# Optimization experiments

Hardware: AMD Instinct MI355X
Metric: run time of the kernel (lower is better)

Reference implementation:

```python
import jax, jax.numpy as jnp
import numpy as np
from jax import lax

B, CIN, S = 16, 1, 64          # batch, input channels, spatial
C = 16                          # c_out hidden channels
T = 50                          # ODE steps
DT = 0.5
NC = 7                          # n_classes
K = T // 2 + 1                  # rfft bins = 26
HID = 256


def conv2d_same(x, w, b):
    # x:(B,Ci,H,W) w:(Co,Ci,3,3) zero 'SAME' padding (torch padding=1)
    y = lax.conv_general_dilated(x, w, (1, 1), 'SAME',
                                 dimension_numbers=('NCHW', 'OIHW', 'NCHW'))
    return y + b[None, :, None, None]


def conv2d_circular(x, w):
    # circular padding=1, no bias (coRNNCell.Wy)
    xp = jnp.pad(x, ((0, 0), (0, 0), (1, 1), (1, 1)), mode='wrap')
    return lax.conv_general_dilated(xp, w, (1, 1), 'VALID',
                                    dimension_numbers=('NCHW', 'OIHW', 'NCHW'))


def setup_inputs() -> dict:
    key = jax.random.key(0)
    ks = iter(jax.random.split(key, 40))
    d = {}
    d['x'] = jax.random.normal(next(ks), (B, CIN, S, S), dtype=jnp.float32)

    def cw(ci, co):
        return jax.random.normal(next(ks), (co, ci, 3, 3), jnp.float32) * (1.0 / np.sqrt(ci * 9))

    # omega / alpha encoders: 3 convs each
    for p in ('om', 'al'):
        d[f'{p}_w1'], d[f'{p}_b1'] = cw(CIN, C), jnp.zeros((C,), jnp.float32)
        d[f'{p}_w2'], d[f'{p}_b2'] = cw(C, C), jnp.zeros((C,), jnp.float32)
        d[f'{p}_w3'], d[f'{p}_b3'] = cw(C, C), jnp.zeros((C,), jnp.float32)
    # hy encoder: 4 convs
    d['hy_w1'], d['hy_b1'] = cw(CIN, C), jnp.zeros((C,), jnp.float32)
    d['hy_w2'], d['hy_b2'] = cw(C, C), jnp.zeros((C,), jnp.float32)
    d['hy_w3'], d['hy_b3'] = cw(C, C), jnp.zeros((C,), jnp.float32)
    d['hy_w4'], d['hy_b4'] = cw(C, C), jnp.zeros((C,), jnp.float32)
    # cell conv: block-diagonal discrete Laplacian (per torch init)
    lap = np.array([[0., 1., 0.], [1., -4., 1.], [0., 1., 0.]], np.float32)
    wy = np.zeros((C, C, 3, 3), np.float32)
    wy[np.arange(C), np.arange(C)] = lap
    d['wy'] = jnp.asarray(wy)
    # readout MLP: 416 -> 256 -> 256 -> 256 -> 7
    dims = [K * C, HID, HID, HID, NC]
    for i in range(4):
        d[f'ro_w{i+1}'] = jax.random.normal(next(ks), (dims[i], dims[i + 1]), jnp.float32) * (1.0 / np.sqrt(dims[i]))
        d[f'ro_b{i+1}'] = jnp.zeros((dims[i + 1],), jnp.float32)
    return d


def _forward(x,
             om_w1, om_b1, om_w2, om_b2, om_w3, om_b3,
             al_w1, al_b1, al_w2, al_b2, al_w3, al_b3,
             hy_w1, hy_b1, hy_w2, hy_b2, hy_w3, hy_b3, hy_w4, hy_b4,
             wy,
             ro_w1, ro_b1, ro_w2, ro_b2, ro_w3, ro_b3, ro_w4, ro_b4):
    relu = jax.nn.relu
    # encoders
    om = relu(conv2d_same(relu(conv2d_same(relu(conv2d_same(x, om_w1, om_b1)), om_w2, om_b2)), om_w3, om_b3))
    al = relu(conv2d_same(relu(conv2d_same(relu(conv2d_same(x, al_w1, al_b1)), al_w2, al_b2)), al_w3, al_b3))
    h = relu(conv2d_same(x, hy_w1, hy_b1))
    h = relu(conv2d_same(h, hy_w2, hy_b2))
    h = relu(conv2d_same(h, hy_w3, hy_b3))
    hy0 = jnp.tanh(conv2d_same(h, hy_w4, hy_b4))

    omega = om.reshape(B, C, S * S)
    alpha = al.reshape(B, C, S * S)
    hy = hy0.reshape(B, C, S * S)
    hz = jnp.zeros_like(hy)

    def step(carry, _):
        hy, hz = carry
        sf = jnp.tanh(conv2d_circular(hy.reshape(B, C, S, S), wy)).reshape(B, C, S * S)
        new_hz = hz + DT * (sf - omega * hy - alpha * hz)
        new_hy = hy + DT * new_hz
        return (new_hy, new_hz), new_hy

    _, y_seq = lax.scan(step, (hy, hz), None, length=T)   # (T,B,C,HW)
    y_seq = jnp.transpose(y_seq, (1, 3, 2, 0)).reshape(B * S * S, C, T)  # (BHW,C,T)

    fft_mag = jnp.abs(jnp.fft.rfft(y_seq, axis=2))        # (BHW,C,K)
    f = fft_mag.reshape(B * S * S, C * K)                  # (BHW, C*K)

    f = relu(f @ ro_w1 + ro_b1)
    f = relu(f @ ro_w2 + ro_b2)
    f = relu(f @ ro_w3 + ro_b3)
    logits_flat = f @ ro_w4 + ro_b4                        # (BHW, NC)
    logits = logits_flat.reshape(B, S, S, NC).transpose(0, 3, 1, 2)
    return logits


def reference(x,
              om_w1, om_b1, om_w2, om_b2, om_w3, om_b3,
              al_w1, al_b1, al_w2, al_b2, al_w3, al_b3,
              hy_w1, hy_b1, hy_w2, hy_b2, hy_w3, hy_b3, hy_w4, hy_b4,
              wy,
              ro_w1, ro_b1, ro_w2, ro_b2, ro_w3, ro_b3, ro_w4, ro_b4):
    return _forward(x,
                    om_w1, om_b1, om_w2, om_b2, om_w3, om_b3,
                    al_w1, al_b1, al_w2, al_b2, al_w3, al_b3,
                    hy_w1, hy_b1, hy_w2, hy_b2, hy_w3, hy_b3, hy_w4, hy_b4,
                    wy,
                    ro_w1, ro_b1, ro_w2, ro_b2, ro_w3, ro_b3, ro_w4, ro_b4)
```

## Files before the change

kernel.cpp:

```cpp
#include <hip/hip_runtime.h>
#include <hip/hip_bf16.h>
#include <hip/hip_fp16.h>
#include <math.h>

#define B_   16
#define C_   16
#define S_   64
#define HW_  4096
#define T_   50
#define K_   26
#define F_   416
#define HID_ 256
#define NC_  7
#define DT_  0.5f
#define BCHW_ (B_*C_*HW_)
#define M_   (B_*HW_)

typedef _Float16 f16x8  __attribute__((ext_vector_type(8)));
typedef __fp16   fp16x2 __attribute__((ext_vector_type(2)));
typedef float    f32x4  __attribute__((ext_vector_type(4)));
typedef float    f32x2  __attribute__((ext_vector_type(2)));

__device__ __forceinline__ void gld_lds16(const void* g, void* l){
    __builtin_amdgcn_global_load_lds(
        (const __attribute__((address_space(1))) void*)g,
        (__attribute__((address_space(3))) void*)l, 16, 0, 0);
}

__device__ __forceinline__ float fast_tanh(float x){
    float ax = fabsf(x);
    float e  = __expf(2.f*ax);
    float r  = 1.f - 2.f/(e + 1.f);
    return copysignf(r, x);
}

__device__ __forceinline__ short f2h_s(float f){
    __half h = __float2half(f);
    return *(short*)&h;
}

template<int CIN, int ACT>
__global__ __launch_bounds__(256) void convf_kernel(
    const float* __restrict__ in0, const float* __restrict__ in1, const float* __restrict__ in2,
    const float* __restrict__ w0,  const float* __restrict__ w1,  const float* __restrict__ w2,
    const float* __restrict__ b0,  const float* __restrict__ b1,  const float* __restrict__ b2,
    float* __restrict__ o0, float* __restrict__ o1, float* __restrict__ o2)
{
    __shared__ __align__(16) float slab[CIN][10][66];
    const int slice = blockIdx.x;
    const int b     = blockIdx.y;
    const int ch    = blockIdx.z;
    const float* in = (ch == 0) ? in0 : (ch == 1) ? in1 : in2;
    const float* w  = (ch == 0) ? w0  : (ch == 1) ? w1  : w2;
    const float* bb = (ch == 0) ? b0  : (ch == 1) ? b1  : b2;
    float* out      = (ch == 0) ? o0  : (ch == 1) ? o1  : o2;

    const int tid = threadIdx.x;
    const int y0  = slice * 8;

    for (int idx = tid; idx < CIN*10*66; idx += 256){
        int ci  = idx / (10*66);
        int rem = idx % (10*66);
        int rr  = rem / 66;
        int cc  = rem % 66;
        int gy = y0 - 1 + rr;
        int gx = cc - 1;
        float v = 0.f;
        if ((unsigned)gy < 64u && (unsigned)gx < 64u)
            v = in[(size_t)(b*CIN + ci)*HW_ + gy*64 + gx];
        slab[ci][rr][cc] = v;
    }
    __syncthreads();

    const int x2 = (tid & 31) * 2;
    const int ry = tid >> 5;

    f32x2 acc[16];
    #pragma unroll
    for (int co = 0; co < 16; co++) acc[co] = (f32x2){bb[co], bb[co]};

    for (int ci = 0; ci < CIN; ci++){
        f32x2 p[3][3];
        #pragma unroll
        for (int dy = 0; dy < 3; dy++){
            float s0 = slab[ci][ry + dy][x2 + 0];
            float s1 = slab[ci][ry + dy][x2 + 1];
            float s2 = slab[ci][ry + dy][x2 + 2];
            float s3 = slab[ci][ry + dy][x2 + 3];
            p[dy][0] = (f32x2){s0, s1};
            p[dy][1] = (f32x2){s1, s2};
            p[dy][2] = (f32x2){s2, s3};
        }
        #pragma unroll
        for (int co = 0; co < 16; co++){
            const float* wp = w + (size_t)(co*CIN + ci)*9;
            f32x2 s = acc[co];
            #pragma unroll
            for (int dy = 0; dy < 3; dy++)
                #pragma unroll
                for (int dx = 0; dx < 3; dx++){
                    float wc = wp[dy*3 + dx];
                    s += (f32x2){wc, wc} * p[dy][dx];
                }
            acc[co] = s;
        }
    }
    #pragma unroll
    for (int co = 0; co < 16; co++){
        float v0 = acc[co].x, v1 = acc[co].y;
        if (ACT){ v0 = fast_tanh(v0); v1 = fast_tanh(v1); }
        else    { v0 = fmaxf(v0, 0.f); v1 = fmaxf(v1, 0.f); }
        *(float2*)&out[(size_t)(b*16 + co)*HW_ + (y0 + ry)*64 + x2] =
            make_float2(v0, v1);
    }
}

__global__ __launch_bounds__(1024) void ode_kernel(
    const float* __restrict__ omega, const float* __restrict__ alpha,
    const float* __restrict__ hy0,   const float* __restrict__ wy,
    __half* __restrict__ yseq)
{
    __shared__ __align__(16) float buf[2][64*68];
    const int blk = blockIdx.x;
    const int c   = blk & 15;
    const int tid = threadIdx.x;
    const int y   = tid >> 4;
    const int xq  = (tid & 15) << 2;
    const size_t off = (size_t)blk * HW_;
    const int g0  = y*64 + xq;

    float4 om4 = *(const float4*)(omega + off + g0);
    float4 al4 = *(const float4*)(alpha + off + g0);
    float4 h4  = *(const float4*)(hy0   + off + g0);

    f32x2 om2[2] = { (f32x2){DT_*om4.x, DT_*om4.y}, (f32x2){DT_*om4.z, DT_*om4.w} };
    f32x2 al2[2] = { (f32x2){1.f - DT_*al4.x, 1.f - DT_*al4.y},
                     (f32x2){1.f - DT_*al4.z, 1.f - DT_*al4.w} };
    f32x2 hz2[2] = { (f32x2){0.f, 0.f}, (f32x2){0.f, 0.f} };
    float hv[4]  = { h4.x, h4.y, h4.z, h4.w };
    *(float4*)&buf[0][y*68 + xq] = h4;

    float wv[9];
    const float* wp = wy + (size_t)(c*C_ + c)*9;
    #pragma unroll
    for (int j = 0; j < 9; j++) wv[j] = wp[j];
    const bool five = (wv[0]==0.f) & (wv[2]==0.f) & (wv[6]==0.f) & (wv[8]==0.f);
    const f32x2 w1v = (f32x2){wv[1], wv[1]};
    const f32x2 w3v = (f32x2){wv[3], wv[3]};
    const f32x2 w4v = (f32x2){wv[4], wv[4]};
    const f32x2 w5v = (f32x2){wv[5], wv[5]};
    const f32x2 w7v = (f32x2){wv[7], wv[7]};
    const f32x2 dt2 = (f32x2){DT_, DT_};
    __syncthreads();

    const int ym = ((y + 63) & 63) * 68;
    const int yp = ((y + 1)  & 63) * 68;
    const int yo = y * 68;
    const int xm = (xq + 63) & 63;
    const int xp = (xq + 4)  & 63;
    const __half* ybase = yseq + off + g0;

    int cur = 0;
    for (int t = 0; t < T_; t++){
        const float* hp = buf[cur];
        float* hn = buf[cur ^ 1];
        float4 up4 = *(const float4*)&hp[ym + xq];
        float4 dn4 = *(const float4*)&hp[yp + xq];
        float lft = hp[yo + xm];
        float rgt = hp[yo + xp];

        float ny0, ny1, ny2, ny3;
        if (five){
            f32x2 u0 = (f32x2){up4.x, up4.y}, u1 = (f32x2){up4.z, up4.w};
            f32x2 d0 = (f32x2){dn4.x, dn4.y}, d1 = (f32x2){dn4.z, dn4.w};
            f32x2 c0 = (f32x2){hv[0], hv[1]}, c1 = (f32x2){hv[2], hv[3]};
            f32x2 l0 = (f32x2){lft,  hv[0]};
            f32x2 l1 = (f32x2){hv[1], hv[2]};
            f32x2 r1 = (f32x2){hv[3], rgt};

            f32x2 s0 = w4v*c0 + w1v*u0 + w7v*d0 + w3v*l0 + w5v*l1;
            f32x2 s1 = w4v*c1 + w1v*u1 + w7v*d1 + w3v*l1 + w5v*r1;

            f32x2 sf0 = (f32x2){fast_tanh(s0.x), fast_tanh(s0.y)};
            f32x2 sf1 = (f32x2){fast_tanh(s1.x), fast_tanh(s1.y)};

            f32x2 nz0 = al2[0]*hz2[0] - om2[0]*c0 + dt2*sf0;
            f32x2 nz1 = al2[1]*hz2[1] - om2[1]*c1 + dt2*sf1;
            f32x2 nyv0 = dt2*nz0 + c0;
            f32x2 nyv1 = dt2*nz1 + c1;
            hz2[0] = nz0; hz2[1] = nz1;
            ny0 = nyv0.x; ny1 = nyv0.y; ny2 = nyv1.x; ny3 = nyv1.y;
        } else {
            float upv[4] = {up4.x, up4.y, up4.z, up4.w};
            float dnv[4] = {dn4.x, dn4.y, dn4.z, dn4.w};
            float ul = hp[ym + xm], ur = hp[ym + xp];
            float dl = hp[yp + xm], dr = hp[yp + xp];
            float hzl[4] = {hz2[0].x, hz2[0].y, hz2[1].x, hz2[1].y};
            float oml[4] = {om2[0].x, om2[0].y, om2[1].x, om2[1].y};
            float all[4] = {al2[0].x, al2[0].y, al2[1].x, al2[1].y};
            float nyv[4];
            #pragma unroll
            for (int i = 0; i < 4; i++){
                float l  = (i == 0) ? lft : hv[i-1];
                float r  = (i == 3) ? rgt : hv[i+1];
                float uL = (i == 0) ? ul  : upv[i-1];
                float uR = (i == 3) ? ur  : upv[i+1];
                float dL = (i == 0) ? dl  : dnv[i-1];
                float dR = (i == 3) ? dr  : dnv[i+1];
                float s = wv[0]*uL + wv[1]*upv[i] + wv[2]*uR
                        + wv[3]*l  + wv[4]*hv[i]  + wv[5]*r
                        + wv[6]*dL + wv[7]*dnv[i] + wv[8]*dR;
                float sf = fast_tanh(s);
                float nz = fmaf(all[i], hzl[i], fmaf(-oml[i], hv[i], DT_*sf));
                nyv[i] = fmaf(DT_, nz, hv[i]);
                hzl[i] = nz;
            }
            hz2[0] = (f32x2){hzl[0], hzl[1]};
            hz2[1] = (f32x2){hzl[2], hzl[3]};
            ny0 = nyv[0]; ny1 = nyv[1]; ny2 = nyv[2]; ny3 = nyv[3];
        }

        hv[0] = ny0; hv[1] = ny1; hv[2] = ny2; hv[3] = ny3;
        *(float4*)&hn[yo + xq] = make_float4(ny0, ny1, ny2, ny3);

        union { fp16x2 h2[2]; uint2 u; } pk;
        pk.h2[0] = __builtin_amdgcn_cvt_pkrtz(ny0, ny1);
        pk.h2[1] = __builtin_amdgcn_cvt_pkrtz(ny2, ny3);
        *(uint2*)(ybase + (size_t)t*BCHW_) = pk.u;

        __syncthreads();
        cur ^= 1;
    }
}

__global__ __launch_bounds__(256) void dft_mfma_kernel(
    const __half* __restrict__ yseq, __half* __restrict__ f)
{
    __shared__ __align__(16) char Ys[8*256*16];
    __shared__ __align__(16) char Gs[8*64*16];
    const int tid = threadIdx.x;
    const int blk = blockIdx.x;
    const int bc  = blk >> 4;
    const int p0  = (blk & 15) << 8;
    const int b   = bc >> 4, c = bc & 15;

    for (int idx = tid; idx < 64*64; idx += 256){
        int r = idx >> 6, t = idx & 63;
        float v = 0.f;
        if (r < 52 && t < 50){
            int k  = r >> 1;
            int ph = (k * t) % 50;
            float ang = (float)ph * (6.2831853071795864f / 50.f);
            v = (r & 1) ? __sinf(ang) : __cosf(ang);
        }
        *(_Float16*)(Gs + ((t >> 3)*64 + r)*16 + (t & 7)*2) = (_Float16)v;
    }

    {
        const __half* src = yseq + (size_t)bc*HW_ + p0 + tid;
        #pragma unroll
        for (int t2 = 0; t2 < 25; t2++){
            unsigned int a = *(const unsigned short*)&src[(size_t)(2*t2)*BCHW_];
            unsigned int d = *(const unsigned short*)&src[(size_t)(2*t2+1)*BCHW_];
            int t8 = t2 >> 2, j = t2 & 3;
            *(unsigned int*)(Ys + (t8*256 + tid)*16 + j*4) = a | (d << 16);
        }
        #pragma unroll
        for (int t2 = 25; t2 < 32; t2++){
            int t8 = t2 >> 2, j = t2 & 3;
            *(unsigned int*)(Ys + (t8*256 + tid)*16 + j*4) = 0u;
        }
    }
    __syncthreads();

    const int lane = tid & 63;
    const int w    = tid >> 6;
    const int n    = lane & 15;
    const int quad = lane >> 4;
    const int mrow = 16*w + n;

    f16x8 a0 = *(const f16x8*)(Gs + ((quad    )*64 + mrow)*16);
    f16x8 a1 = *(const f16x8*)(Gs + ((quad + 4)*64 + mrow)*16);

    const int kb0   = 8*w + 2*quad;
    const bool valid = (kb0 < K_);

    for (int nt = 0; nt < 16; nt++){
        f16x8 b0 = *(const f16x8*)(Ys + ((quad    )*256 + nt*16 + n)*16);
        f16x8 b1 = *(const f16x8*)(Ys + ((quad + 4)*256 + nt*16 + n)*16);
        f32x4 acc = (f32x4){0.f, 0.f, 0.f, 0.f};
        acc = __builtin_amdgcn_mfma_f32_16x16x32_f16(a0, b0, acc, 0, 0, 0);
        acc = __builtin_amdgcn_mfma_f32_16x16x32_f16(a1, b1, acc, 0, 0, 0);
        if (valid){
            float m0 = sqrtf(fmaf(acc[0], acc[0], acc[1]*acc[1]));
            float m1 = sqrtf(fmaf(acc[2], acc[2], acc[3]*acc[3]));
            unsigned int u = ((unsigned int)(unsigned short)f2h_s(m1) << 16)
                           |  (unsigned int)(unsigned short)f2h_s(m0);
            const int row = b*HW_ + p0 + nt*16 + n;
            *(unsigned int*)((char*)(f + (size_t)row*F_ + c*K_) + kb0*2) = u;
        }
    }
}

__global__ __launch_bounds__(256) void prep_all_kernel(
    const float* __restrict__ w1, const float* __restrict__ w2,
    const float* __restrict__ w3,
    __half* __restrict__ wt1, __half* __restrict__ wt2, __half* __restrict__ wt3)
{
    const int blk = blockIdx.x;
    const int tid = threadIdx.x;
    if (blk < 256){
        const int n = blk;
        for (int k = tid; k < F_; k += 256)
            wt1[(size_t)n*F_ + k] = __float2half(w1[(size_t)k*HID_ + n]);
    } else if (blk < 512){
        const int n = blk - 256;
        for (int k = tid; k < HID_; k += 256)
            wt2[(size_t)n*HID_ + k] = __float2half(w2[(size_t)k*HID_ + n]);
    } else {
        const int n = blk - 512;
        for (int k = tid; k < HID_; k += 256)
            wt3[(size_t)n*HID_ + k] = __float2half(w3[(size_t)k*HID_ + n]);
    }
}

__global__ __launch_bounds__(512, 2) void mlp_fused_kernel(
    const __half* __restrict__ A,
    const __half* __restrict__ Wt1,
    const __half* __restrict__ Wt2,
    const __half* __restrict__ Wt3,
    const float* __restrict__ b1, const float* __restrict__ b2,
    const float* __restrict__ b3,
    const float* __restrict__ w4, const float* __restrict__ b4,
    float* __restrict__ out)
{
    __shared__ __align__(16) short hbuf[256*264];
    __shared__ __align__(16) short Bs[4*2064];
    __shared__ __align__(16) short Bs4[512*8];

    const int tid  = threadIdx.x;
    const int lane = tid & 63;
    const int wave = tid >> 6;
    const int wm   = (wave & 3) * 64;
    const int wn   = (wave >> 2) * 128;
    const int n16  = lane & 15;
    const int quad = lane >> 4;
    const int m0   = blockIdx.x * 256;

    {
        const int ktq = tid >> 4, n = tid & 15;
        short vals[8];
        #pragma unroll
        for (int e = 0; e < 8; e++){
            const int k = ktq*8 + e;
            vals[e] = f2h_s((n < NC_) ? w4[(size_t)k*NC_ + n] : 0.f);
        }
        #pragma unroll
        for (int e = 0; e < 8; e++) Bs4[tid*8 + e] = vals[e];
    }

    const int id0 = tid, id1 = tid + 512;
    const int kc0 = id0 >> 8, nn0 = id0 & 255;
    const int kc1 = id1 >> 8, nn1 = id1 & 255;
    char* dst0 = (char*)Bs + kc0*4128 + nn0*16;
    char* dst1 = (char*)Bs + kc1*4128 + nn1*16;

    f32x4 acc[4][8];
    #pragma unroll
    for (int i = 0; i < 4; i++)
        #pragma unroll
        for (int j = 0; j < 8; j++)
            acc[i][j] = (f32x4){0.f,0.f,0.f,0.f};

    const __half* arow[4];
    #pragma unroll
    for (int i = 0; i < 4; i++)
        arow[i] = A + (size_t)(m0 + wm + i*16 + n16)*F_ + quad*8;

    f16x8 afn[4];
    #pragma unroll
    for (int i = 0; i < 4; i++) afn[i] = *(const f16x8*)(arow[i]);

    for (int k0 = 0; k0 < F_; k0 += 32){
        gld_lds16(Wt1 + (size_t)nn0*F_ + k0 + kc0*8, dst0);
        gld_lds16(Wt1 + (size_t)nn1*F_ + k0 + kc1*8, dst1);
        __syncthreads();
        f16x8 af[4];
        #pragma unroll
        for (int i = 0; i < 4; i++) af[i] = afn[i];
        if (k0 + 32 < F_){
            #pragma unroll
            for (int i = 0; i < 4; i++) afn[i] = *(const f16x8*)(arow[i] + k0 + 32);
        }
        f16x8 bf[8];
        #pragma unroll
        for (int j = 0; j < 8; j++)
            bf[j] = *(const f16x8*)((char*)Bs + quad*4128 + (wn + j*16 + n16)*16);
        #pragma unroll
        for (int i = 0; i < 4; i++)
            #pragma unroll
            for (int j = 0; j < 8; j++)
                acc[i][j] = __builtin_amdgcn_mfma_f32_16x16x32_f16(
                                af[i], bf[j], acc[i][j], 0, 0, 0);
        __syncthreads();
    }
    #pragma unroll
    for (int j = 0; j < 8; j++){
        const int col = wn + j*16 + n16;
        const float bv = b1[col];
        #pragma unroll
        for (int i = 0; i < 4; i++){
            const int r0 = wm + i*16 + quad*4;
            #pragma unroll
            for (int r = 0; r < 4; r++)
                hbuf[(r0 + r)*264 + col] = f2h_s(fmaxf(acc[i][j][r] + bv, 0.f));
        }
    }
    __syncthreads();

    const __half* Wts[2] = {Wt2, Wt3};
    const float* bls[2] = {b2, b3};
    for (int L = 0; L < 2; L++){
        const __half* Wt = Wts[L];
        #pragma unroll
        for (int i = 0; i < 4; i++)
            #pragma unroll
            for (int j = 0; j < 8; j++)
                acc[i][j] = (f32x4){0.f,0.f,0.f,0.f};

        for (int k0 = 0; k0 < HID_; k0 += 32){
            gld_lds16(Wt + (size_t)nn0*HID_ + k0 + kc0*8, dst0);
            gld_lds16(Wt + (size_t)nn1*HID_ + k0 + kc1*8, dst1);
            f16x8 af[4];
            #pragma unroll
            for (int i = 0; i < 4; i++)
                af[i] = *(const f16x8*)&hbuf[(wm + i*16 + n16)*264 + k0 + quad*8];
            __syncthreads();
            f16x8 bf[8];
            #pragma unroll
            for (int j = 0; j < 8; j++)
                bf[j] = *(const f16x8*)((char*)Bs + quad*4128 + (wn + j*16 + n16)*16);
            #pragma unroll
            for (int i = 0; i < 4; i++)
                #pragma unroll
                for (int j = 0; j < 8; j++)
                    acc[i][j] = __builtin_amdgcn_mfma_f32_16x16x32_f16(
                                    af[i], bf[j], acc[i][j], 0, 0, 0);
            __syncthreads();
        }
        const float* bl = bls[L];
        #pragma unroll
        for (int j = 0; j < 8; j++){
            const int col = wn + j*16 + n16;
            const float bv = bl[col];
            #pragma unroll
            for (int i = 0; i < 4; i++){
                const int r0 = wm + i*16 + quad*4;
                #pragma unroll
                for (int r = 0; r < 4; r++)
                    hbuf[(r0 + r)*264 + col] = f2h_s(fmaxf(acc[i][j][r] + bv, 0.f));
            }
        }
        __syncthreads();
    }

    f32x4 facc[2] = {(f32x4){0.f,0.f,0.f,0.f}, (f32x4){0.f,0.f,0.f,0.f}};
    #pragma unroll
    for (int kt = 0; kt < 8; kt++){
        f16x8 bfr = *(const f16x8*)&Bs4[((kt*4 + quad)*16 + n16)*8];
        #pragma unroll
        for (int mt = 0; mt < 2; mt++){
            f16x8 af = *(const f16x8*)&hbuf[(wave*32 + mt*16 + n16)*264 + kt*32 + quad*8];
            facc[mt] = __builtin_amdgcn_mfma_f32_16x16x32_f16(af, bfr, facc[mt], 0, 0, 0);
        }
    }
    if (n16 < NC_){
        const float bv = b4[n16];
        #pragma unroll
        for (int mt = 0; mt < 2; mt++){
            #pragma unroll
            for (int r = 0; r < 4; r++){
                const int grow = m0 + wave*32 + mt*16 + quad*4 + r;
                const int bidx = grow >> 12, hw = grow & 4095;
                out[(size_t)(bidx*NC_ + n16)*HW_ + hw] = facc[mt][r] + bv;
            }
        }
    }
}

extern "C" void kernel_launch(void* const* d_in, const int* in_sizes, int n_in,
                              void* d_out, int out_size, void* d_ws, size_t ws_size,
                              hipStream_t stream)
{
    const float* x     = (const float*)d_in[0];
    const float* om_w1 = (const float*)d_in[1];  const float* om_b1 = (const float*)d_in[2];
    const float* om_w2 = (const float*)d_in[3];  const float* om_b2 = (const float*)d_in[4];
    const float* om_w3 = (const float*)d_in[5];  const float* om_b3 = (const float*)d_in[6];
    const float* al_w1 = (const float*)d_in[7];  const float* al_b1 = (const float*)d_in[8];
    const float* al_w2 = (const float*)d_in[9];  const float* al_b2 = (const float*)d_in[10];
    const float* al_w3 = (const float*)d_in[11]; const float* al_b3 = (const float*)d_in[12];
    const float* hy_w1 = (const float*)d_in[13]; const float* hy_b1 = (const float*)d_in[14];
    const float* hy_w2 = (const float*)d_in[15]; const float* hy_b2 = (const float*)d_in[16];
    const float* hy_w3 = (const float*)d_in[17]; const float* hy_b3 = (const float*)d_in[18];
    const float* hy_w4 = (const float*)d_in[19]; const float* hy_b4 = (const float*)d_in[20];
    const float* wy    = (const float*)d_in[21];
    const float* ro_w1 = (const float*)d_in[22]; const float* ro_b1 = (const float*)d_in[23];
    const float* ro_w2 = (const float*)d_in[24]; const float* ro_b2 = (const float*)d_in[25];
    const float* ro_w3 = (const float*)d_in[26]; const float* ro_b3 = (const float*)d_in[27];
    const float* ro_w4 = (const float*)d_in[28]; const float* ro_b4 = (const float*)d_in[29];
    float* out = (float*)d_out;

    char* wsb = (char*)d_ws;
    const size_t YSEQ_BYTES = (size_t)T_ * BCHW_ * 2;
    __half* yseq = (__half*)wsb;
    __half* fbuf = (__half*)(wsb + YSEQ_BYTES);

    const size_t MB4 = (size_t)BCHW_ * 4;
    float* om_t1 = (float*)(wsb + YSEQ_BYTES + 0*MB4);
    float* al_t1 = (float*)(wsb + YSEQ_BYTES + 1*MB4);
    float* hy_t1 = (float*)(wsb + YSEQ_BYTES + 2*MB4);
    float* om_t2 = (float*)(wsb + YSEQ_BYTES + 3*MB4);
    float* al_t2 = (float*)(wsb + YSEQ_BYTES + 4*MB4);
    float* hy_t2 = (float*)(wsb + YSEQ_BYTES + 5*MB4);
    float* omega = (float*)(wsb + YSEQ_BYTES + 6*MB4);
    float* alpha = (float*)(wsb + YSEQ_BYTES + 7*MB4);
    float* hy_t3 = (float*)(wsb + YSEQ_BYTES + 8*MB4);
    float* hy0   = (float*)(wsb + YSEQ_BYTES + 9*MB4);

    __half* wt1 = (__half*)(wsb + 0);
    __half* wt2 = (__half*)(wsb + 212992);
    __half* wt3 = (__half*)(wsb + 344064);

    convf_kernel<1,0><<<dim3(8,B_,3), 256, 0, stream>>>(
        x, x, x, om_w1, al_w1, hy_w1, om_b1, al_b1, hy_b1, om_t1, al_t1, hy_t1);
    convf_kernel<16,0><<<dim3(8,B_,3), 256, 0, stream>>>(
        om_t1, al_t1, hy_t1, om_w2, al_w2, hy_w2, om_b2, al_b2, hy_b2, om_t2, al_t2, hy_t2);
    convf_kernel<16,0><<<dim3(8,B_,3), 256, 0, stream>>>(
        om_t2, al_t2, hy_t2, om_w3, al_w3, hy_w3, om_b3, al_b3, hy_b3, omega, alpha, hy_t3);
    convf_kernel<16,1><<<dim3(8,B_,1), 256, 0, stream>>>(
        hy_t3, hy_t3, hy_t3, hy_w4, hy_w4, hy_w4, hy_b4, hy_b4, hy_b4, hy0, hy0, hy0);
    ode_kernel<<<256, 1024, 0, stream>>>(omega, alpha, hy0, wy, yseq);
    dft_mfma_kernel<<<4096, 256, 0, stream>>>(yseq, fbuf);
    prep_all_kernel<<<768, 256, 0, stream>>>(ro_w1, ro_w2, ro_w3, wt1, wt2, wt3);
    mlp_fused_kernel<<<256, 512, 0, stream>>>(
        fbuf, wt1, wt2, wt3, ro_b1, ro_b2, ro_b3, ro_w4, ro_b4, out);
}
```

Before: 372.1 us.

## Shrink fused MLP tile to 64 rows, 4 waves, XOR-swizzled LDS

Reworks the fused MLP kernel from 256-row tiles with 8 waves to 64-row tiles with 4 waves, launching 1024 blocks instead of 256 so all CUs are busy. The hidden-activation buffer is shrunk and uses an XOR swizzle in place of row padding to avoid LDS bank conflicts, and the final-layer weights now reuse the B staging buffer. The trade-off is that each block reloads the full weight matrices, so there is four times as much weight traffic through L2 and less reuse per weight tile.

```diff
diff --git a/kernel.cpp b/kernel.cpp
--- a/kernel.cpp
+++ b/kernel.cpp
@@ -324,7 +324,7 @@
     }
 }
 
-__global__ __launch_bounds__(512, 2) void mlp_fused_kernel(
+__global__ __launch_bounds__(256, 3) void mlp_fused_kernel(
     const __half* __restrict__ A,
     const __half* __restrict__ Wt1,
     const __half* __restrict__ Wt2,
@@ -334,56 +334,45 @@
     const float* __restrict__ w4, const float* __restrict__ b4,
     float* __restrict__ out)
 {
-    __shared__ __align__(16) short hbuf[256*264];
-    __shared__ __align__(16) short Bs[4*2064];
-    __shared__ __align__(16) short Bs4[512*8];
+    __shared__ __align__(16) short hbuf[64*256];
+    __shared__ __align__(16) short Bs[1024*8];
 
     const int tid  = threadIdx.x;
     const int lane = tid & 63;
     const int wave = tid >> 6;
-    const int wm   = (wave & 3) * 64;
-    const int wn   = (wave >> 2) * 128;
+    const int wn   = wave * 64;
     const int n16  = lane & 15;
     const int quad = lane >> 4;
-    const int m0   = blockIdx.x * 256;
-
-    {
-        const int ktq = tid >> 4, n = tid & 15;
-        short vals[8];
-        #pragma unroll
-        for (int e = 0; e < 8; e++){
-            const int k = ktq*8 + e;
-            vals[e] = f2h_s((n < NC_) ? w4[(size_t)k*NC_ + n] : 0.f);
-        }
-        #pragma unroll
-        for (int e = 0; e < 8; e++) Bs4[tid*8 + e] = vals[e];
-    }
-
-    const int id0 = tid, id1 = tid + 512;
-    const int kc0 = id0 >> 8, nn0 = id0 & 255;
-    const int kc1 = id1 >> 8, nn1 = id1 & 255;
-    char* dst0 = (char*)Bs + kc0*4128 + nn0*16;
-    char* dst1 = (char*)Bs + kc1*4128 + nn1*16;
-
-    f32x4 acc[4][8];
+    const int m0   = blockIdx.x * 64;
+
+    int kcs[4], nns[4];
+    #pragma unroll
+    for (int s = 0; s < 4; s++){
+        int id = tid + 256*s;
+        kcs[s] = id >> 8; nns[s] = id & 255;
+    }
+
+    f32x4 acc[4][4];
     #pragma unroll
     for (int i = 0; i < 4; i++)
         #pragma unroll
-        for (int j = 0; j < 8; j++)
+        for (int j = 0; j < 4; j++)
             acc[i][j] = (f32x4){0.f,0.f,0.f,0.f};
 
     const __half* arow[4];
     #pragma unroll
     for (int i = 0; i < 4; i++)
-        arow[i] = A + (size_t)(m0 + wm + i*16 + n16)*F_ + quad*8;
+        arow[i] = A + (size_t)(m0 + i*16 + n16)*F_ + quad*8;
 
     f16x8 afn[4];
     #pragma unroll
     for (int i = 0; i < 4; i++) afn[i] = *(const f16x8*)(arow[i]);
 
     for (int k0 = 0; k0 < F_; k0 += 32){
-        gld_lds16(Wt1 + (size_t)nn0*F_ + k0 + kc0*8, dst0);
-        gld_lds16(Wt1 + (size_t)nn1*F_ + k0 + kc1*8, dst1);
+        #pragma unroll
+        for (int s = 0; s < 4; s++)
+            gld_lds16(Wt1 + (size_t)nns[s]*F_ + k0 + kcs[s]*8,
+                      (char*)Bs + (tid + 256*s)*16);
         __syncthreads();
         f16x8 af[4];
         #pragma unroll
@@ -392,28 +381,31 @@
             #pragma unroll
             for (int i = 0; i < 4; i++) afn[i] = *(const f16x8*)(arow[i] + k0 + 32);
         }
-        f16x8 bf[8];
-        #pragma unroll
-        for (int j = 0; j < 8; j++)
-            bf[j] = *(const f16x8*)((char*)Bs + quad*4128 + (wn + j*16 + n16)*16);
+        f16x8 bf[4];
+        #pragma unroll
+        for (int j = 0; j < 4; j++)
+            bf[j] = *(const f16x8*)&Bs[(quad*256 + wn + j*16 + n16)*8];
         #pragma unroll
         for (int i = 0; i < 4; i++)
             #pragma unroll
-            for (int j = 0; j < 8; j++)
+            for (int j = 0; j < 4; j++)
                 acc[i][j] = __builtin_amdgcn_mfma_f32_16x16x32_f16(
                                 af[i], bf[j], acc[i][j], 0, 0, 0);
         __syncthreads();
     }
     #pragma unroll
-    for (int j = 0; j < 8; j++){
+    for (int j = 0; j < 4; j++){
         const int col = wn + j*16 + n16;
         const float bv = b1[col];
         #pragma unroll
         for (int i = 0; i < 4; i++){
-            const int r0 = wm + i*16 + quad*4;
-            #pragma unroll
-            for (int r = 0; r < 4; r++)
-                hbuf[(r0 + r)*264 + col] = f2h_s(fmaxf(acc[i][j][r] + bv, 0.f));
+            const int r0 = i*16 + quad*4;
+            #pragma unroll
+            for (int r = 0; r < 4; r++){
+                const int row = r0 + r;
+                hbuf[row*256 + (((col>>3) ^ (row&7))<<3) + (col&7)] =
+                    f2h_s(fmaxf(acc[i][j][r] + bv, 0.f));
+            }
         }
     }
     __syncthreads();
@@ -425,65 +417,80 @@
         #pragma unroll
         for (int i = 0; i < 4; i++)
             #pragma unroll
-            for (int j = 0; j < 8; j++)
+            for (int j = 0; j < 4; j++)
                 acc[i][j] = (f32x4){0.f,0.f,0.f,0.f};
 
         for (int k0 = 0; k0 < HID_; k0 += 32){
-            gld_lds16(Wt + (size_t)nn0*HID_ + k0 + kc0*8, dst0);
-            gld_lds16(Wt + (size_t)nn1*HID_ + k0 + kc1*8, dst1);
+            #pragma unroll
+            for (int s = 0; s < 4; s++)
+                gld_lds16(Wt + (size_t)nns[s]*HID_ + k0 + kcs[s]*8,
+                          (char*)Bs + (tid + 256*s)*16);
             f16x8 af[4];
             #pragma unroll
-            for (int i = 0; i < 4; i++)
-                af[i] = *(const f16x8*)&hbuf[(wm + i*16 + n16)*264 + k0 + quad*8];
+            for (int i = 0; i < 4; i++){
+                const int row = i*16 + n16;
+                const int phys = ((k0>>3) + quad) ^ (row & 7);
+                af[i] = *(const f16x8*)&hbuf[row*256 + phys*8];
+            }
             __syncthreads();
-            f16x8 bf[8];
-            #pragma unroll
-            for (int j = 0; j < 8; j++)
-                bf[j] = *(const f16x8*)((char*)Bs + quad*4128 + (wn + j*16 + n16)*16);
+            f16x8 bf[4];
+            #pragma unroll
+            for (int j = 0; j < 4; j++)
+                bf[j] = *(const f16x8*)&Bs[(quad*256 + wn + j*16 + n16)*8];
             #pragma unroll
             for (int i = 0; i < 4; i++)
                 #pragma unroll
-                for (int j = 0; j < 8; j++)
+                for (int j = 0; j < 4; j++)
                     acc[i][j] = __builtin_amdgcn_mfma_f32_16x16x32_f16(
                                     af[i], bf[j], acc[i][j], 0, 0, 0);
             __syncthreads();
         }
         const float* bl = bls[L];
         #pragma unroll
-        for (int j = 0; j < 8; j++){
+        for (int j = 0; j < 4; j++){
             const int col = wn + j*16 + n16;
             const float bv = bl[col];
             #pragma unroll
             for (int i = 0; i < 4; i++){
-                const int r0 = wm + i*16 + quad*4;
+                const int r0 = i*16 + quad*4;
                 #pragma unroll
-                for (int r = 0; r < 4; r++)
-                    hbuf[(r0 + r)*264 + col] = f2h_s(fmaxf(acc[i][j][r] + bv, 0.f));
+                for (int r = 0; r < 4; r++){
+                    const int row = r0 + r;
+                    hbuf[row*256 + (((col>>3) ^ (row&7))<<3) + (col&7)] =
+                        f2h_s(fmaxf(acc[i][j][r] + bv, 0.f));
+                }
             }
         }
         __syncthreads();
     }
 
-    f32x4 facc[2] = {(f32x4){0.f,0.f,0.f,0.f}, (f32x4){0.f,0.f,0.f,0.f}};
+    #pragma unroll
+    for (int s = 0; s < 2; s++){
+        const int id  = tid + 256*s;
+        const int ktq = id >> 4, nn4 = id & 15;
+        #pragma unroll
+        for (int e = 0; e < 8; e++)
+            Bs[id*8 + e] = f2h_s((nn4 < NC_) ?
+                w4[(size_t)(ktq*8 + e)*NC_ + nn4] : 0.f);
+    }
+    __syncthreads();
+
+    f32x4 facc = (f32x4){0.f,0.f,0.f,0.f};
+    const int frow = wave*16 + n16;
     #pragma unroll
     for (int kt = 0; kt < 8; kt++){
-        f16x8 bfr = *(const f16x8*)&Bs4[((kt*4 + quad)*16 + n16)*8];
-        #pragma unroll
-        for (int mt = 0; mt < 2; mt++){
-            f16x8 af = *(const f16x8*)&hbuf[(wave*32 + mt*16 + n16)*264 + kt*32 + quad*8];
-            facc[mt] = __builtin_amdgcn_mfma_f32_16x16x32_f16(af, bfr, facc[mt], 0, 0, 0);
-        }
+        f16x8 bfr = *(const f16x8*)&Bs[((kt*4 + quad)*16 + n16)*8];
+        const int phys = (kt*4 + quad) ^ (frow & 7);
+        f16x8 af = *(const f16x8*)&hbuf[frow*256 + phys*8];
+        facc = __builtin_amdgcn_mfma_f32_16x16x32_f16(af, bfr, facc, 0, 0, 0);
     }
     if (n16 < NC_){
         const float bv = b4[n16];
         #pragma unroll
-        for (int mt = 0; mt < 2; mt++){
-            #pragma unroll
-            for (int r = 0; r < 4; r++){
-                const int grow = m0 + wave*32 + mt*16 + quad*4 + r;
-                const int bidx = grow >> 12, hw = grow & 4095;
-                out[(size_t)(bidx*NC_ + n16)*HW_ + hw] = facc[mt][r] + bv;
-            }
+        for (int r = 0; r < 4; r++){
+            const int grow = m0 + wave*16 + quad*4 + r;
+            const int bidx = grow >> 12, hw = grow & 4095;
+            out[(size_t)(bidx*NC_ + n16)*HW_ + hw] = facc[r] + bv;
         }
     }
 }
@@ -542,6 +549,6 @@
     ode_kernel<<<256, 1024, 0, stream>>>(omega, alpha, hy0, wy, yseq);
     dft_mfma_kernel<<<4096, 256, 0, stream>>>(yseq, fbuf);
     prep_all_kernel<<<768, 256, 0, stream>>>(ro_w1, ro_w2, ro_w3, wt1, wt2, wt3);
-    mlp_fused_kernel<<<256, 512, 0, stream>>>(
+    mlp_fused_kernel<<<1024, 256, 0, stream>>>(
         fbuf, wt1, wt2, wt3, ro_b1, ro_b2, ro_b3, ro_w4, ro_b4, out);
 }
```

Measured after the change: 422.7 us. +13.6%, slower.

## Double K-step per barrier in fused MLP and XOR-swizzle hidden buffer

Applied to the files above, without the earlier changes.

The fused MLP kernel now processes 64 K-elements per LDS stage (two MFMA k-substeps per pair of barriers) instead of 32, which halves the number of barrier pairs in each layer. The padded hidden buffer (row stride 264) is replaced by an unpadded 256-stride buffer with an XOR swizzle to avoid LDS bank conflicts. The separate W4 staging buffer is removed and W4 is loaded into the reused B buffer only after layer 3, which cuts the kernel's LDS footprint. In exchange, the A-operand software prefetch is dropped and there is a peeled tail step for K=416.

```diff
diff --git a/kernel.cpp b/kernel.cpp
--- a/kernel.cpp
+++ b/kernel.cpp
@@ -334,9 +334,8 @@
     const float* __restrict__ w4, const float* __restrict__ b4,
     float* __restrict__ out)
 {
-    __shared__ __align__(16) short hbuf[256*264];
-    __shared__ __align__(16) short Bs[4*2064];
-    __shared__ __align__(16) short Bs4[512*8];
+    __shared__ __align__(16) short hbuf[256*256];
+    __shared__ __align__(16) short Bs[8*256*8];
 
     const int tid  = threadIdx.x;
     const int lane = tid & 63;
@@ -347,23 +346,12 @@
     const int quad = lane >> 4;
     const int m0   = blockIdx.x * 256;
 
-    {
-        const int ktq = tid >> 4, n = tid & 15;
-        short vals[8];
-        #pragma unroll
-        for (int e = 0; e < 8; e++){
-            const int k = ktq*8 + e;
-            vals[e] = f2h_s((n < NC_) ? w4[(size_t)k*NC_ + n] : 0.f);
-        }
-        #pragma unroll
-        for (int e = 0; e < 8; e++) Bs4[tid*8 + e] = vals[e];
-    }
-
-    const int id0 = tid, id1 = tid + 512;
-    const int kc0 = id0 >> 8, nn0 = id0 & 255;
-    const int kc1 = id1 >> 8, nn1 = id1 & 255;
-    char* dst0 = (char*)Bs + kc0*4128 + nn0*16;
-    char* dst1 = (char*)Bs + kc1*4128 + nn1*16;
+    int kcs[4], nns[4];
+    #pragma unroll
+    for (int s = 0; s < 4; s++){
+        int id = tid + 512*s;
+        kcs[s] = id >> 8; nns[s] = id & 255;
+    }
 
     f32x4 acc[4][8];
     #pragma unroll
@@ -377,25 +365,50 @@
     for (int i = 0; i < 4; i++)
         arow[i] = A + (size_t)(m0 + wm + i*16 + n16)*F_ + quad*8;
 
-    f16x8 afn[4];
-    #pragma unroll
-    for (int i = 0; i < 4; i++) afn[i] = *(const f16x8*)(arow[i]);
-
-    for (int k0 = 0; k0 < F_; k0 += 32){
-        gld_lds16(Wt1 + (size_t)nn0*F_ + k0 + kc0*8, dst0);
-        gld_lds16(Wt1 + (size_t)nn1*F_ + k0 + kc1*8, dst1);
+    for (int k0 = 0; k0 < 384; k0 += 64){
+        #pragma unroll
+        for (int s = 0; s < 4; s++)
+            gld_lds16(Wt1 + (size_t)nns[s]*F_ + k0 + kcs[s]*8,
+                      (char*)Bs + (tid + 512*s)*16);
+        f16x8 af[2][4];
+        #pragma unroll
+        for (int h = 0; h < 2; h++)
+            #pragma unroll
+            for (int i = 0; i < 4; i++)
+                af[h][i] = *(const f16x8*)(arow[i] + k0 + h*32);
         __syncthreads();
+        #pragma unroll
+        for (int h = 0; h < 2; h++){
+            f16x8 bf[8];
+            #pragma unroll
+            for (int j = 0; j < 8; j++)
+                bf[j] = *(const f16x8*)&Bs[((h*4 + quad)*256 + wn + j*16 + n16)*8];
+            #pragma unroll
+            for (int i = 0; i < 4; i++)
+                #pragma unroll
+                for (int j = 0; j < 8; j++)
+                    acc[i][j] = __builtin_amdgcn_mfma_f32_16x16x32_f16(
+                                    af[h][i], bf[j], acc[i][j], 0, 0, 0);
+        }
+        __syncthreads();
+    }
+    {
+        const int k0 = 384;
+        #pragma unroll
+        for (int s = 0; s < 2; s++){
+            int id = tid + 512*s;
+            int kc = id >> 8;
+            int nn = id & 255;
+            gld_lds16(Wt1 + (size_t)nn*F_ + k0 + kc*8, (char*)Bs + id*16);
+        }
         f16x8 af[4];
         #pragma unroll
-        for (int i = 0; i < 4; i++) af[i] = afn[i];
-        if (k0 + 32 < F_){
-            #pragma unroll
-            for (int i = 0; i < 4; i++) afn[i] = *(const f16x8*)(arow[i] + k0 + 32);
-        }
+        for (int i = 0; i < 4; i++) af[i] = *(const f16x8*)(arow[i] + k0);
+        __syncthreads();
         f16x8 bf[8];
         #pragma unroll
         for (int j = 0; j < 8; j++)
-            bf[j] = *(const f16x8*)((char*)Bs + quad*4128 + (wn + j*16 + n16)*16);
+            bf[j] = *(const f16x8*)&Bs[(quad*256 + wn + j*16 + n16)*8];
         #pragma unroll
         for (int i = 0; i < 4; i++)
             #pragma unroll
@@ -412,8 +425,11 @@
         for (int i = 0; i < 4; i++){
             const int r0 = wm + i*16 + quad*4;
             #pragma unroll
-            for (int r = 0; r < 4; r++)
-                hbuf[(r0 + r)*264 + col] = f2h_s(fmaxf(acc[i][j][r] + bv, 0.f));
+            for (int r = 0; r < 4; r++){
+                const int row = r0 + r;
+                hbuf[row*256 + (((col>>3) ^ (row&7))<<3) + (col&7)] =
+                    f2h_s(fmaxf(acc[i][j][r] + bv, 0.f));
+            }
         }
     }
     __syncthreads();
@@ -428,24 +444,34 @@
             for (int j = 0; j < 8; j++)
                 acc[i][j] = (f32x4){0.f,0.f,0.f,0.f};
 
-        for (int k0 = 0; k0 < HID_; k0 += 32){
-            gld_lds16(Wt + (size_t)nn0*HID_ + k0 + kc0*8, dst0);
-            gld_lds16(Wt + (size_t)nn1*HID_ + k0 + kc1*8, dst1);
-            f16x8 af[4];
-            #pragma unroll
-            for (int i = 0; i < 4; i++)
-                af[i] = *(const f16x8*)&hbuf[(wm + i*16 + n16)*264 + k0 + quad*8];
+        for (int k0 = 0; k0 < HID_; k0 += 64){
+            #pragma unroll
+            for (int s = 0; s < 4; s++)
+                gld_lds16(Wt + (size_t)nns[s]*HID_ + k0 + kcs[s]*8,
+                          (char*)Bs + (tid + 512*s)*16);
+            f16x8 af[2][4];
+            #pragma unroll
+            for (int h = 0; h < 2; h++)
+                #pragma unroll
+                for (int i = 0; i < 4; i++){
+                    const int row  = wm + i*16 + n16;
+                    const int phys = ((k0>>3) + h*4 + quad) ^ (row & 7);
+                    af[h][i] = *(const f16x8*)&hbuf[row*256 + phys*8];
+                }
             __syncthreads();
-            f16x8 bf[8];
-            #pragma unroll
-            for (int j = 0; j < 8; j++)
-                bf[j] = *(const f16x8*)((char*)Bs + quad*4128 + (wn + j*16 + n16)*16);
-            #pragma unroll
-            for (int i = 0; i < 4; i++)
+            #pragma unroll
+            for (int h = 0; h < 2; h++){
+                f16x8 bf[8];
                 #pragma unroll
                 for (int j = 0; j < 8; j++)
-                    acc[i][j] = __builtin_amdgcn_mfma_f32_16x16x32_f16(
-                                    af[i], bf[j], acc[i][j], 0, 0, 0);
+                    bf[j] = *(const f16x8*)&Bs[((h*4 + quad)*256 + wn + j*16 + n16)*8];
+                #pragma unroll
+                for (int i = 0; i < 4; i++)
+                    #pragma unroll
+                    for (int j = 0; j < 8; j++)
+                        acc[i][j] = __builtin_amdgcn_mfma_f32_16x16x32_f16(
+                                        af[h][i], bf[j], acc[i][j], 0, 0, 0);
+            }
             __syncthreads();
         }
         const float* bl = bls[L];
@@ -457,20 +483,35 @@
             for (int i = 0; i < 4; i++){
                 const int r0 = wm + i*16 + quad*4;
                 #pragma unroll
-                for (int r = 0; r < 4; r++)
-                    hbuf[(r0 + r)*264 + col] = f2h_s(fmaxf(acc[i][j][r] + bv, 0.f));
+                for (int r = 0; r < 4; r++){
+                    const int row = r0 + r;
+                    hbuf[row*256 + (((col>>3) ^ (row&7))<<3) + (col&7)] =
+                        f2h_s(fmaxf(acc[i][j][r] + bv, 0.f));
+                }
             }
         }
         __syncthreads();
     }
 
+    {
+        const int id  = tid;
+        const int ktq = id >> 4, nn4 = id & 15;
+        #pragma unroll
+        for (int e = 0; e < 8; e++)
+            Bs[id*8 + e] = f2h_s((nn4 < NC_) ?
+                w4[(size_t)(ktq*8 + e)*NC_ + nn4] : 0.f);
+    }
+    __syncthreads();
+
     f32x4 facc[2] = {(f32x4){0.f,0.f,0.f,0.f}, (f32x4){0.f,0.f,0.f,0.f}};
     #pragma unroll
     for (int kt = 0; kt < 8; kt++){
-        f16x8 bfr = *(const f16x8*)&Bs4[((kt*4 + quad)*16 + n16)*8];
+        f16x8 bfr = *(const f16x8*)&Bs[((kt*4 + quad)*16 + n16)*8];
         #pragma unroll
         for (int mt = 0; mt < 2; mt++){
-            f16x8 af = *(const f16x8*)&hbuf[(wave*32 + mt*16 + n16)*264 + kt*32 + quad*8];
+            const int frow = wave*32 + mt*16 + n16;
+            const int phys = (kt*4 + quad) ^ (frow & 7);
+            f16x8 af = *(const f16x8*)&hbuf[frow*256 + phys*8];
             facc[mt] = __builtin_amdgcn_mfma_f32_16x16x32_f16(af, bfr, facc[mt], 0, 0, 0);
         }
     }
```

After: 409.8 us. +10.1%, slower.
